# Kernel optimization log

Hardware: AMD Instinct MI355X
Metric: run time of the kernel (lower is better)

The kernel has to match this reference:

```python
import jax, jax.numpy as jnp
import numpy as np

D_MODEL = 1024
N_HEADS = 16
HEAD_DIM = D_MODEL // N_HEADS
B, LQ, LK = 4, 2048, 2048


def _rope(x, cos, sin):
    # x: (B, H, L, d); cos/sin: (B, 1, L, d)
    d = x.shape[-1]
    x1, x2 = x[..., : d // 2], x[..., d // 2 :]
    rotated = jnp.concatenate([-x2, x1], axis=-1)
    return x * cos + rotated * sin


def setup_inputs() -> dict:
    key = jax.random.key(0)
    ks = jax.random.split(key, 16)
    s = 1.0 / np.sqrt(D_MODEL)
    inp = {
        "query": jax.random.normal(ks[0], (B, LQ, D_MODEL), jnp.float32),
        "key": jax.random.normal(ks[1], (B, LK, D_MODEL), jnp.float32),
        "value": jax.random.normal(ks[2], (B, LK, D_MODEL), jnp.float32),
        "cos_q": jax.random.normal(ks[3], (B, LQ, HEAD_DIM), jnp.float32),
        "sin_q": jax.random.normal(ks[4], (B, LQ, HEAD_DIM), jnp.float32),
        "cos_k": jax.random.normal(ks[5], (B, LK, HEAD_DIM), jnp.float32),
        "sin_k": jax.random.normal(ks[6], (B, LK, HEAD_DIM), jnp.float32),
        "key_padding_mask": jnp.zeros((B, LK), dtype=bool),
        "Wq": jax.random.normal(ks[7], (D_MODEL, D_MODEL), jnp.float32) * s,
        "bq": jnp.zeros((D_MODEL,), jnp.float32),
        "Wk": jax.random.normal(ks[8], (D_MODEL, D_MODEL), jnp.float32) * s,
        "bk": jnp.zeros((D_MODEL,), jnp.float32),
        "Wv": jax.random.normal(ks[9], (D_MODEL, D_MODEL), jnp.float32) * s,
        "bv": jnp.zeros((D_MODEL,), jnp.float32),
        "Wo": jax.random.normal(ks[10], (D_MODEL, D_MODEL), jnp.float32) * s,
        "bo": jnp.zeros((D_MODEL,), jnp.float32),
    }
    return inp


def reference(query, key, value, cos_q, sin_q, cos_k, sin_k, key_padding_mask,
              Wq, bq, Wk, bk, Wv, bv, Wo, bo):
    Bq, Lq, _ = query.shape
    Lk = key.shape[1]
    scale = HEAD_DIM ** -0.5

    def proj(x, W, b, L):
        # torch Linear: x @ W.T + b, then (B, L, H, d) -> (B, H, L, d)
        y = jnp.einsum('ble,de->bld', x, W) + b
        return y.reshape(Bq, L, N_HEADS, HEAD_DIM).transpose(0, 2, 1, 3)

    q = proj(query, Wq, bq, Lq)
    k = proj(key, Wk, bk, Lk)
    v = proj(value, Wv, bv, Lk)

    q = _rope(q, cos_q[:, None, :Lq, :HEAD_DIM], sin_q[:, None, :Lq, :HEAD_DIM])
    k = _rope(k, cos_k[:, None, :Lk, :HEAD_DIM], sin_k[:, None, :Lk, :HEAD_DIM])

    attn = jnp.einsum('bhqd,bhkd->bhqk', q, k) * scale
    attn = jnp.where(key_padding_mask[:, None, None, :], -jnp.inf, attn)
    attn = jax.nn.softmax(attn, axis=-1)

    out = jnp.einsum('bhqk,bhkd->bhqd', attn, v)
    out = out.transpose(0, 2, 1, 3).reshape(Bq, Lq, D_MODEL)
    return jnp.einsum('ble,de->bld', out, Wo) + bo
```

## Files before the change

kernel.cpp:

```cpp
#include <hip/hip_runtime.h>
#include <hip/hip_bf16.h>
#include <stdint.h>
#include <stddef.h>

#define B_DIM 4
#define NH    16
#define LSEQ  2048
#define HD    64
#define DM    1024
#define TOKENS (B_DIM * LSEQ)

typedef __bf16 bf16_t;
typedef __attribute__((ext_vector_type(8))) __bf16 bf16x8;
typedef __attribute__((ext_vector_type(4))) __bf16 bf16x4;
typedef __attribute__((ext_vector_type(4))) float  f32x4;

#define GLD16(gp, lp) \
  __builtin_amdgcn_global_load_lds((__attribute__((address_space(1))) void*)(gp), \
                                   (__attribute__((address_space(3))) void*)(lp), 16, 0, 0)

#define WAITV4 asm volatile("s_waitcnt vmcnt(4)" ::: "memory")
#define WAITV0 asm volatile("s_waitcnt vmcnt(0)" ::: "memory")
#define WAITL0 asm volatile("s_waitcnt lgkmcnt(0)" ::: "memory")
#define SBAR   __builtin_amdgcn_s_barrier()
#define SCHED0 __builtin_amdgcn_sched_barrier(0)

__device__ __forceinline__ f32x4 mfma_16x16x32(bf16x8 a, bf16x8 b, f32x4 c) {
  return __builtin_amdgcn_mfma_f32_16x16x32_bf16(a, b, c, 0, 0, 0);
}

__global__ __launch_bounds__(256) void cast3_kernel(const float* __restrict__ a,
                                                    const float* __restrict__ b,
                                                    const float* __restrict__ c,
                                                    bf16_t* __restrict__ dst, int n) {
  const float* src = (blockIdx.y == 0) ? a : (blockIdx.y == 1) ? b : c;
  const int i = (blockIdx.x * 256 + threadIdx.x) * 4;
  if (i < n) {
    const float4 v = *(const float4*)(src + i);
    bf16x4 o;
    o[0] = (bf16_t)v.x; o[1] = (bf16_t)v.y; o[2] = (bf16_t)v.z; o[3] = (bf16_t)v.w;
    *(bf16x4*)(dst + (size_t)blockIdx.y * n + i) = o;
  }
}

__global__ __launch_bounds__(256) void cast4_kernel(const float* __restrict__ a,
                                                    const float* __restrict__ b,
                                                    const float* __restrict__ c,
                                                    const float* __restrict__ d,
                                                    bf16_t* __restrict__ dst, int n) {
  const float* src = (blockIdx.y == 0) ? a : (blockIdx.y == 1) ? b
                   : (blockIdx.y == 2) ? c : d;
  const int i = (blockIdx.x * 256 + threadIdx.x) * 4;
  if (i < n) {
    const float4 v = *(const float4*)(src + i);
    bf16x4 o;
    o[0] = (bf16_t)v.x; o[1] = (bf16_t)v.y; o[2] = (bf16_t)v.z; o[3] = (bf16_t)v.w;
    *(bf16x4*)(dst + (size_t)blockIdx.y * n + i) = o;
  }
}

#define GEMM_TILE(CUR, WAIT, PRE, KK2)                                        \
  {                                                                           \
    WAIT; SBAR; SCHED0;                                                       \
    const bf16_t* Ac = &As[CUR][0];                                           \
    const bf16_t* Bc = &Bs[CUR][0];                                           \
    bf16x8 af[4], bfr[4];                                                     \
    _Pragma("unroll") for (int i_ = 0; i_ < 4; ++i_)                          \
      af[i_] = *(const bf16x8*)(Ac + (wm + i_ * 16 + l16) * 32 + fcol);       \
    _Pragma("unroll") for (int j_ = 0; j_ < 4; ++j_)                          \
      bfr[j_] = *(const bf16x8*)(Bc + (wn + j_ * 16 + l16) * 32 + fcol);      \
    _Pragma("unroll") for (int i_ = 0; i_ < 4; ++i_)                          \
      _Pragma("unroll") for (int j_ = 0; j_ < 4; ++j_)                        \
        acc[i_][j_] = mfma_16x16x32(af[i_], bfr[j_], acc[i_][j_]);            \
    WAITL0; SBAR; SCHED0;                                                     \
    if (PRE) {                                                                \
      const int kk2_ = (KK2);                                                 \
      GLD16(Ag0 + kk2_, &As[CUR][0] + ld0);                                   \
      GLD16(Ag1 + kk2_, &As[CUR][0] + ld1);                                   \
      GLD16(Bg0 + kk2_, &Bs[CUR][0] + ld0);                                   \
      GLD16(Bg1 + kk2_, &Bs[CUR][0] + ld1);                                   \
    }                                                                         \
  }

__global__ __launch_bounds__(256) void qkv_proj_kernel(const bf16_t* __restrict__ X,
                                                       const bf16_t* __restrict__ Wb,
                                                       const float* __restrict__ bq,
                                                       const float* __restrict__ bk,
                                                       const float* __restrict__ bv,
                                                       const float* __restrict__ cos_q,
                                                       const float* __restrict__ sin_q,
                                                       const float* __restrict__ cos_k,
                                                       const float* __restrict__ sin_k,
                                                       bf16_t* __restrict__ qtb,
                                                       bf16_t* __restrict__ ktb,
                                                       bf16_t* __restrict__ vtb) {
  __shared__ bf16_t As[2][128 * 32];
  __shared__ bf16_t Bs[2][128 * 32];
  const int z = blockIdx.z;
  const bf16_t* A  = X  + (size_t)z * TOKENS * DM;
  const bf16_t* Bw = Wb + (size_t)z * DM * DM;
  const float* bias = (z == 0) ? bq : (z == 1) ? bk : bv;

  const int tid  = threadIdx.x;
  const int wave = tid >> 6, lane = tid & 63;
  const int quad = lane >> 4, l16 = lane & 15;
  const int m0 = blockIdx.x * 128, n0 = blockIdx.y * 128;
  const int wm = (wave >> 1) * 64, wn = (wave & 1) * 64;

  f32x4 acc[4][4];
#pragma unroll
  for (int i = 0; i < 4; ++i)
#pragma unroll
    for (int j = 0; j < 4; ++j) acc[i][j] = (f32x4){0.f, 0.f, 0.f, 0.f};

  const int srow = lane >> 2;
  const int scol = ((lane & 3) ^ ((lane >> 3) & 3)) * 8;
  const int c0 = wave * 2, c1 = c0 + 1;
  const int r0 = c0 * 16 + srow, r1 = c1 * 16 + srow;
  const bf16_t* Ag0 = A  + (size_t)(m0 + r0) * DM + scol;
  const bf16_t* Ag1 = A  + (size_t)(m0 + r1) * DM + scol;
  const bf16_t* Bg0 = Bw + (size_t)(n0 + r0) * DM + scol;
  const bf16_t* Bg1 = Bw + (size_t)(n0 + r1) * DM + scol;
  const int ld0 = c0 * 512, ld1 = c1 * 512;

  const int fcol = ((quad ^ ((l16 >> 1) & 3)) << 3);

  GLD16(Ag0, &As[0][0] + ld0); GLD16(Ag1, &As[0][0] + ld1);
  GLD16(Bg0, &Bs[0][0] + ld0); GLD16(Bg1, &Bs[0][0] + ld1);
  GLD16(Ag0 + 32, &As[1][0] + ld0); GLD16(Ag1 + 32, &As[1][0] + ld1);
  GLD16(Bg0 + 32, &Bs[1][0] + ld0); GLD16(Bg1 + 32, &Bs[1][0] + ld1);

  for (int ii = 0; ii < 15; ++ii) {
    const int kk2a = ii * 64 + 64;
    GEMM_TILE(0, WAITV4, true, kk2a);
    GEMM_TILE(1, WAITV4, true, kk2a + 32);
  }
  GEMM_TILE(0, WAITV4, false, 0);
  GEMM_TILE(1, WAITV0, false, 0);

  if (z < 2) {
    const float* cosb = (z == 0) ? cos_q : cos_k;
    const float* sinb = (z == 0) ? sin_q : sin_k;
    bf16_t* out = (z == 0) ? qtb : ktb;
    const int h = (n0 + wn) >> 6;
#pragma unroll
    for (int i = 0; i < 4; ++i) {
#pragma unroll
      for (int j = 0; j < 2; ++j) {
        const int hd1 = j * 16 + l16;
        const int hd2 = hd1 + 32;
        const float bn1 = bias[n0 + wn + hd1];
        const float bn2 = bias[n0 + wn + hd2];
#pragma unroll
        for (int r = 0; r < 4; ++r) {
          const int m = m0 + wm + i * 16 + quad * 4 + r;
          const int b = m >> 11, l = m & (LSEQ - 1);
          const size_t cb = ((size_t)b * LSEQ + l) * HD;
          const float x1 = (float)(bf16_t)(acc[i][j][r] + bn1);
          const float x2 = (float)(bf16_t)(acc[i][j + 2][r] + bn2);
          const float c1 = cosb[cb + hd1], s1 = sinb[cb + hd1];
          const float c2 = cosb[cb + hd2], s2 = sinb[cb + hd2];
          bf16_t* dst = out + (((size_t)(b * NH + h)) * LSEQ + l) * HD;
          dst[hd1] = (bf16_t)(x1 * c1 - x2 * s1);
          dst[hd2] = (bf16_t)(x2 * c2 + x1 * s2);
        }
      }
    }
  } else {
#pragma unroll
    for (int i = 0; i < 4; ++i) {
      const int mb = m0 + wm + i * 16 + quad * 4;
      const int b = mb >> 11, l = mb & (LSEQ - 1);
#pragma unroll
      for (int j = 0; j < 4; ++j) {
        const int n = n0 + wn + j * 16 + l16;
        const int h = n >> 6, hd = n & (HD - 1);
        const float bn = bias[n];
        bf16x4 pk;
#pragma unroll
        for (int r = 0; r < 4; ++r) pk[r] = (bf16_t)(acc[i][j][r] + bn);
        *(bf16x4*)(vtb + (((size_t)(b * NH + h)) * HD + hd) * LSEQ + l) = pk;
      }
    }
  }
}

__global__ __launch_bounds__(256) void out_gemm_kernel(const bf16_t* __restrict__ A,
                                                       const bf16_t* __restrict__ Bw,
                                                       const float* __restrict__ bias,
                                                       float* __restrict__ out) {
  __shared__ bf16_t As[2][128 * 32];
  __shared__ bf16_t Bs[2][128 * 32];
  const int tid  = threadIdx.x;
  const int wave = tid >> 6, lane = tid & 63;
  const int quad = lane >> 4, l16 = lane & 15;
  const int m0 = blockIdx.x * 128, n0 = blockIdx.y * 128;
  const int wm = (wave >> 1) * 64, wn = (wave & 1) * 64;

  f32x4 acc[4][4];
#pragma unroll
  for (int i = 0; i < 4; ++i)
#pragma unroll
    for (int j = 0; j < 4; ++j) acc[i][j] = (f32x4){0.f, 0.f, 0.f, 0.f};

  const int srow = lane >> 2;
  const int scol = ((lane & 3) ^ ((lane >> 3) & 3)) * 8;
  const int c0 = wave * 2, c1 = c0 + 1;
  const int r0 = c0 * 16 + srow, r1 = c1 * 16 + srow;
  const bf16_t* Ag0 = A  + (size_t)(m0 + r0) * DM + scol;
  const bf16_t* Ag1 = A  + (size_t)(m0 + r1) * DM + scol;
  const bf16_t* Bg0 = Bw + (size_t)(n0 + r0) * DM + scol;
  const bf16_t* Bg1 = Bw + (size_t)(n0 + r1) * DM + scol;
  const int ld0 = c0 * 512, ld1 = c1 * 512;
  const int fcol = ((quad ^ ((l16 >> 1) & 3)) << 3);

  GLD16(Ag0, &As[0][0] + ld0); GLD16(Ag1, &As[0][0] + ld1);
  GLD16(Bg0, &Bs[0][0] + ld0); GLD16(Bg1, &Bs[0][0] + ld1);
  GLD16(Ag0 + 32, &As[1][0] + ld0); GLD16(Ag1 + 32, &As[1][0] + ld1);
  GLD16(Bg0 + 32, &Bs[1][0] + ld0); GLD16(Bg1 + 32, &Bs[1][0] + ld1);

  for (int ii = 0; ii < 15; ++ii) {
    const int kk2a = ii * 64 + 64;
    GEMM_TILE(0, WAITV4, true, kk2a);
    GEMM_TILE(1, WAITV4, true, kk2a + 32);
  }
  GEMM_TILE(0, WAITV4, false, 0);
  GEMM_TILE(1, WAITV0, false, 0);

#pragma unroll
  for (int i = 0; i < 4; ++i)
#pragma unroll
    for (int j = 0; j < 4; ++j) {
      const int n  = n0 + wn + j * 16 + l16;
      const float bn = bias[n];
#pragma unroll
      for (int r = 0; r < 4; ++r) {
        const int m = m0 + wm + i * 16 + quad * 4 + r;
        out[(size_t)m * DM + n] = acc[i][j][r] + bn;
      }
    }
}

__global__ __launch_bounds__(256, 4) void attn_kernel(const bf16_t* __restrict__ qt,
                                                      const bf16_t* __restrict__ kt,
                                                      const bf16_t* __restrict__ vt,
                                                      const unsigned char* __restrict__ mask,
                                                      bf16_t* __restrict__ ctx) {
  __shared__ bf16_t Kl[2][64 * 64];
  __shared__ bf16_t Vl[2][64 * 64];
  __shared__ int mflag;
  const int bh = blockIdx.y;
  const int b = bh >> 4, h = bh & (NH - 1);
  const int q0 = blockIdx.x * 128;
  const int tid = threadIdx.x;
  const int wave = tid >> 6, lane = tid & 63;
  const int quad = lane >> 4, l16 = lane & 15;
  const float scale_l2e = 0.125f * 1.44269504f;

  const bf16_t* kbase = kt + (size_t)bh * LSEQ * HD;
  const bf16_t* vbase = vt + (size_t)bh * HD * LSEQ;
  const unsigned char* mrow = mask + (size_t)b * LSEQ;

  if (tid == 0) mflag = 0;
  __syncthreads();
  {
    const uint64_t mw = ((const uint64_t*)mrow)[tid];
    if (mw != 0) atomicOr(&mflag, 1);
  }

  bf16x8 qa[2][2];
#pragma unroll
  for (int u = 0; u < 2; ++u) {
    const bf16_t* qrow = qt + (((size_t)bh * LSEQ) + q0 + wave * 32 + u * 16 + l16) * HD;
    qa[u][0] = *(const bf16x8*)(qrow + quad * 8);
    qa[u][1] = *(const bf16x8*)(qrow + 32 + quad * 8);
  }

  f32x4 O[2][4];
  f32x4 Ol[2];
#pragma unroll
  for (int u = 0; u < 2; ++u) {
    Ol[u] = (f32x4){0.f, 0.f, 0.f, 0.f};
#pragma unroll
    for (int j = 0; j < 4; ++j) O[u][j] = (f32x4){0.f, 0.f, 0.f, 0.f};
  }
  bf16x8 ones;
#pragma unroll
  for (int e = 0; e < 8; ++e) ones[e] = (bf16_t)1.0f;

  const int srow8 = lane >> 3;
  const int scb   = lane & 7;
  const int c0 = wave * 2, c1 = c0 + 1;
  const int p0 = c0 * 8 + srow8, p1 = p0 + 8;
  const int g0 = (scb ^ srow8) * 8;
  const int sig0 = ((p0 >> 5) << 5) | (((p0 >> 2) & 3) << 3) | (((p0 >> 4) & 1) << 2) | (p0 & 3);
  const int sig1 = ((p1 >> 5) << 5) | (((p1 >> 2) & 3) << 3) | (((p1 >> 4) & 1) << 2) | (p1 & 3);
  const int kgo0 = sig0 * HD + g0, kgo1 = sig1 * HD + g0;
  const int vgo0 = p0 * LSEQ + g0, vgo1 = p1 * LSEQ + g0;
  const int ld0 = c0 * 512, ld1 = c1 * 512;

  const int sw  = l16 & 7;
  const int oA  = l16 * 64 + ((quad ^ sw) << 3);
  const int oB  = l16 * 64 + (((quad + 4) ^ sw) << 3);

  GLD16(kbase + kgo0, &Kl[0][0] + ld0);
  GLD16(kbase + kgo1, &Kl[0][0] + ld1);
  GLD16(vbase + vgo0, &Vl[0][0] + ld0);
  GLD16(vbase + vgo1, &Vl[0][0] + ld1);
  __syncthreads();
  const bool has_mask = (mflag != 0);

  int cur = 0;
  for (int t = 0; t < 32; ++t) {
    const int k0 = t * 64;

    if (t < 31) {
      const int k0n = k0 + 64;
      bf16_t* Kd = &Kl[cur ^ 1][0];
      bf16_t* Vd = &Vl[cur ^ 1][0];
      GLD16(kbase + (size_t)k0n * HD + kgo0, Kd + ld0);
      GLD16(kbase + (size_t)k0n * HD + kgo1, Kd + ld1);
      GLD16(vbase + (size_t)(vgo0 + k0n), Vd + ld0);
      GLD16(vbase + (size_t)(vgo1 + k0n), Vd + ld1);
    }

    const bf16_t* Kc = &Kl[cur][0];
    const bf16_t* Vc = &Vl[cur][0];

    f32x4 S[2][4];
#pragma unroll
    for (int j = 0; j < 4; ++j) {
      const bf16x8 kb0 = *(const bf16x8*)(Kc + oA + j * 1024);
      const bf16x8 kb1 = *(const bf16x8*)(Kc + oB + j * 1024);
#pragma unroll
      for (int u = 0; u < 2; ++u) {
        f32x4 a = (f32x4){0.f, 0.f, 0.f, 0.f};
        a = mfma_16x16x32(kb0, qa[u][0], a);
        a = mfma_16x16x32(kb1, qa[u][1], a);
#pragma unroll
        for (int r = 0; r < 4; ++r)
          S[u][j][r] = __builtin_amdgcn_exp2f(a[r] * scale_l2e);
      }
    }

    if (has_mask) {
      const uint64_t mlo = *(const uint64_t*)(mrow + k0 + quad * 8);
      const uint64_t mhi = *(const uint64_t*)(mrow + k0 + 32 + quad * 8);
      if (!__all((mlo | mhi) == 0)) {
#pragma unroll
        for (int j = 0; j < 4; ++j) {
          const uint64_t mm = (j & 2) ? mhi : mlo;
#pragma unroll
          for (int r = 0; r < 4; ++r)
            if ((mm >> (((j & 1) * 4 + r) * 8)) & 0xff) {
              S[0][j][r] = 0.f;
              S[1][j][r] = 0.f;
            }
        }
      }
    }

    bf16x8 pa[2][2];
#pragma unroll
    for (int u = 0; u < 2; ++u)
#pragma unroll
      for (int f = 0; f < 2; ++f)
#pragma unroll
        for (int e = 0; e < 8; ++e)
          pa[u][f][e] = (bf16_t)S[u][2 * f + (e >> 2)][e & 3];

#pragma unroll
    for (int u = 0; u < 2; ++u) {
      Ol[u] = mfma_16x16x32(pa[u][0], ones, Ol[u]);
      Ol[u] = mfma_16x16x32(pa[u][1], ones, Ol[u]);
    }

#pragma unroll
    for (int jd = 0; jd < 4; ++jd) {
      const bf16x8 vb0 = *(const bf16x8*)(Vc + oA + jd * 1024);
      const bf16x8 vb1 = *(const bf16x8*)(Vc + oB + jd * 1024);
#pragma unroll
      for (int u = 0; u < 2; ++u) {
        O[u][jd] = mfma_16x16x32(pa[u][0], vb0, O[u][jd]);
        O[u][jd] = mfma_16x16x32(pa[u][1], vb1, O[u][jd]);
      }
    }

    if (t < 31) __syncthreads();
    cur ^= 1;
  }

#pragma unroll
  for (int u = 0; u < 2; ++u) {
    f32x4 linv;
#pragma unroll
    for (int r = 0; r < 4; ++r) linv[r] = 1.0f / Ol[u][r];
#pragma unroll
    for (int jd = 0; jd < 4; ++jd)
#pragma unroll
      for (int r = 0; r < 4; ++r) {
        const int l = q0 + wave * 32 + u * 16 + quad * 4 + r;
        const int d = h * HD + jd * 16 + l16;
        const float o = O[u][jd][r] * linv[r];
        ctx[((size_t)b * LSEQ + l) * DM + d] = (bf16_t)o;
      }
  }
}

extern "C" void kernel_launch(void* const* d_in, const int* in_sizes, int n_in,
                              void* d_out, int out_size, void* d_ws, size_t ws_size,
                              hipStream_t stream) {
  (void)in_sizes; (void)n_in; (void)out_size; (void)ws_size;
  const float* query = (const float*)d_in[0];
  const float* key   = (const float*)d_in[1];
  const float* value = (const float*)d_in[2];
  const float* cos_q = (const float*)d_in[3];
  const float* sin_q = (const float*)d_in[4];
  const float* cos_k = (const float*)d_in[5];
  const float* sin_k = (const float*)d_in[6];
  const unsigned char* mask = (const unsigned char*)d_in[7];
  const float* Wq = (const float*)d_in[8];
  const float* bq = (const float*)d_in[9];
  const float* Wk = (const float*)d_in[10];
  const float* bk = (const float*)d_in[11];
  const float* Wv = (const float*)d_in[12];
  const float* bv = (const float*)d_in[13];
  const float* Wo = (const float*)d_in[14];
  const float* bo = (const float*)d_in[15];
  float* out = (float*)d_out;

  const size_t ACT = (size_t)TOKENS * DM;
  const size_t WEL = (size_t)DM * DM;

  bf16_t* p   = (bf16_t*)d_ws;
  bf16_t* xq  = p; p += ACT;
  bf16_t* xk  = p; p += ACT;
  bf16_t* xv  = p; p += ACT;
  bf16_t* wqb = p; p += WEL;
  bf16_t* wkb = p; p += WEL;
  bf16_t* wvb = p; p += WEL;
  bf16_t* wob = p; p += WEL;
  bf16_t* qtb = p; p += ACT;
  bf16_t* ktb = p; p += ACT;
  bf16_t* vtb = p; p += ACT;
  bf16_t* ctx = xk;
  (void)xv; (void)wkb; (void)wvb;

  cast3_kernel<<<dim3((int)(ACT / 1024), 3), 256, 0, stream>>>(query, key, value, xq, (int)ACT);
  cast4_kernel<<<dim3((int)(WEL / 1024), 4), 256, 0, stream>>>(Wq, Wk, Wv, Wo, wqb, (int)WEL);

  qkv_proj_kernel<<<dim3(TOKENS / 128, DM / 128, 3), 256, 0, stream>>>(
      xq, wqb, bq, bk, bv, cos_q, sin_q, cos_k, sin_k, qtb, ktb, vtb);

  attn_kernel<<<dim3(LSEQ / 128, B_DIM * NH), 256, 0, stream>>>(qtb, ktb, vtb, mask, ctx);

  out_gemm_kernel<<<dim3(TOKENS / 128, DM / 128), 256, 0, stream>>>(ctx, wob, bo, out);
}
```

Before: 359.9 us.

## Triple-buffer GEMM loads, swizzle block order, deepen attention prefetch pipeline

The projection GEMMs move from double to triple buffering in LDS with a vmcnt(8) wait, so global loads run two K-tiles ahead. Block indices in both GEMMs and the attention kernel are remapped so that neighbouring blocks share operand tiles in L2. The attention loop now prefetches two KV tiles ahead and uses explicit vmcnt waits and barriers in place of __syncthreads. The larger LDS footprint in the GEMMs may lower occupancy, and the remapping assumes fixed grid dimensions.

Measured after the change: 363.8 us. No clear change (+1.1%).

```diff
diff --git a/kernel.cpp b/kernel.cpp
--- a/kernel.cpp
+++ b/kernel.cpp
@@ -19,6 +19,7 @@
   __builtin_amdgcn_global_load_lds((__attribute__((address_space(1))) void*)(gp), \
                                    (__attribute__((address_space(3))) void*)(lp), 16, 0, 0)
 
+#define WAITV8 asm volatile("s_waitcnt vmcnt(8)" ::: "memory")
 #define WAITV4 asm volatile("s_waitcnt vmcnt(4)" ::: "memory")
 #define WAITV0 asm volatile("s_waitcnt vmcnt(0)" ::: "memory")
 #define WAITL0 asm volatile("s_waitcnt lgkmcnt(0)" ::: "memory")
@@ -82,6 +83,25 @@
     }                                                                         \
   }
 
+#define GEMM_LOOP                                                             \
+  GLD16(Ag0, &As[0][0] + ld0); GLD16(Ag1, &As[0][0] + ld1);                   \
+  GLD16(Bg0, &Bs[0][0] + ld0); GLD16(Bg1, &Bs[0][0] + ld1);                   \
+  GLD16(Ag0 + 32, &As[1][0] + ld0); GLD16(Ag1 + 32, &As[1][0] + ld1);         \
+  GLD16(Bg0 + 32, &Bs[1][0] + ld0); GLD16(Bg1 + 32, &Bs[1][0] + ld1);         \
+  GLD16(Ag0 + 64, &As[2][0] + ld0); GLD16(Ag1 + 64, &As[2][0] + ld1);         \
+  GLD16(Bg0 + 64, &Bs[2][0] + ld0); GLD16(Bg1 + 64, &Bs[2][0] + ld1);         \
+  for (int ii = 0; ii < 9; ++ii) {                                            \
+    const int kkb = ii * 96 + 96;                                             \
+    GEMM_TILE(0, WAITV8, true, kkb);                                          \
+    GEMM_TILE(1, WAITV8, true, kkb + 32);                                     \
+    GEMM_TILE(2, WAITV8, true, kkb + 64);                                     \
+  }                                                                           \
+  GEMM_TILE(0, WAITV8, true, 960);                                            \
+  GEMM_TILE(1, WAITV8, true, 992);                                            \
+  GEMM_TILE(2, WAITV8, false, 0);                                             \
+  GEMM_TILE(0, WAITV4, false, 0);                                             \
+  GEMM_TILE(1, WAITV0, false, 0);
+
 __global__ __launch_bounds__(256) void qkv_proj_kernel(const bf16_t* __restrict__ X,
                                                        const bf16_t* __restrict__ Wb,
                                                        const float* __restrict__ bq,
@@ -94,8 +114,8 @@
                                                        bf16_t* __restrict__ qtb,
                                                        bf16_t* __restrict__ ktb,
                                                        bf16_t* __restrict__ vtb) {
-  __shared__ bf16_t As[2][128 * 32];
-  __shared__ bf16_t Bs[2][128 * 32];
+  __shared__ bf16_t As[3][128 * 32];
+  __shared__ bf16_t Bs[3][128 * 32];
   const int z = blockIdx.z;
   const bf16_t* A  = X  + (size_t)z * TOKENS * DM;
   const bf16_t* Bw = Wb + (size_t)z * DM * DM;
@@ -104,7 +124,10 @@
   const int tid  = threadIdx.x;
   const int wave = tid >> 6, lane = tid & 63;
   const int quad = lane >> 4, l16 = lane & 15;
-  const int m0 = blockIdx.x * 128, n0 = blockIdx.y * 128;
+  const int L  = blockIdx.x + (blockIdx.y << 6);
+  const int mt = ((L & 7) << 3) | ((L >> 3) & 7);
+  const int nt = L >> 6;
+  const int m0 = mt * 128, n0 = nt * 128;
   const int wm = (wave >> 1) * 64, wn = (wave & 1) * 64;
 
   f32x4 acc[4][4];
@@ -125,18 +148,7 @@
 
   const int fcol = ((quad ^ ((l16 >> 1) & 3)) << 3);
 
-  GLD16(Ag0, &As[0][0] + ld0); GLD16(Ag1, &As[0][0] + ld1);
-  GLD16(Bg0, &Bs[0][0] + ld0); GLD16(Bg1, &Bs[0][0] + ld1);
-  GLD16(Ag0 + 32, &As[1][0] + ld0); GLD16(Ag1 + 32, &As[1][0] + ld1);
-  GLD16(Bg0 + 32, &Bs[1][0] + ld0); GLD16(Bg1 + 32, &Bs[1][0] + ld1);
-
-  for (int ii = 0; ii < 15; ++ii) {
-    const int kk2a = ii * 64 + 64;
-    GEMM_TILE(0, WAITV4, true, kk2a);
-    GEMM_TILE(1, WAITV4, true, kk2a + 32);
-  }
-  GEMM_TILE(0, WAITV4, false, 0);
-  GEMM_TILE(1, WAITV0, false, 0);
+  GEMM_LOOP
 
   if (z < 2) {
     const float* cosb = (z == 0) ? cos_q : cos_k;
@@ -189,12 +201,15 @@
                                                        const bf16_t* __restrict__ Bw,
                                                        const float* __restrict__ bias,
                                                        float* __restrict__ out) {
-  __shared__ bf16_t As[2][128 * 32];
-  __shared__ bf16_t Bs[2][128 * 32];
+  __shared__ bf16_t As[3][128 * 32];
+  __shared__ bf16_t Bs[3][128 * 32];
   const int tid  = threadIdx.x;
   const int wave = tid >> 6, lane = tid & 63;
   const int quad = lane >> 4, l16 = lane & 15;
-  const int m0 = blockIdx.x * 128, n0 = blockIdx.y * 128;
+  const int L  = blockIdx.x + (blockIdx.y << 6);
+  const int mt = ((L & 7) << 3) | ((L >> 3) & 7);
+  const int nt = L >> 6;
+  const int m0 = mt * 128, n0 = nt * 128;
   const int wm = (wave >> 1) * 64, wn = (wave & 1) * 64;
 
   f32x4 acc[4][4];
@@ -214,18 +229,7 @@
   const int ld0 = c0 * 512, ld1 = c1 * 512;
   const int fcol = ((quad ^ ((l16 >> 1) & 3)) << 3);
 
-  GLD16(Ag0, &As[0][0] + ld0); GLD16(Ag1, &As[0][0] + ld1);
-  GLD16(Bg0, &Bs[0][0] + ld0); GLD16(Bg1, &Bs[0][0] + ld1);
-  GLD16(Ag0 + 32, &As[1][0] + ld0); GLD16(Ag1 + 32, &As[1][0] + ld1);
-  GLD16(Bg0 + 32, &Bs[1][0] + ld0); GLD16(Bg1 + 32, &Bs[1][0] + ld1);
-
-  for (int ii = 0; ii < 15; ++ii) {
-    const int kk2a = ii * 64 + 64;
-    GEMM_TILE(0, WAITV4, true, kk2a);
-    GEMM_TILE(1, WAITV4, true, kk2a + 32);
-  }
-  GEMM_TILE(0, WAITV4, false, 0);
-  GEMM_TILE(1, WAITV0, false, 0);
+  GEMM_LOOP
 
 #pragma unroll
   for (int i = 0; i < 4; ++i)
@@ -240,6 +244,55 @@
       }
     }
 }
+
+#define ATTN_TILE(K0)                                                         \
+  {                                                                           \
+    const bf16_t* Kc = &Kl[cur][0];                                           \
+    const bf16_t* Vc = &Vl[cur][0];                                           \
+    f32x4 S[2][4];                                                            \
+    _Pragma("unroll") for (int j = 0; j < 4; ++j) {                           \
+      const bf16x8 kb0 = *(const bf16x8*)(Kc + oA + j * 1024);                \
+      const bf16x8 kb1 = *(const bf16x8*)(Kc + oB + j * 1024);                \
+      _Pragma("unroll") for (int u = 0; u < 2; ++u) {                         \
+        f32x4 a = (f32x4){0.f, 0.f, 0.f, 0.f};                                \
+        a = mfma_16x16x32(kb0, qa[u][0], a);                                  \
+        a = mfma_16x16x32(kb1, qa[u][1], a);                                  \
+        _Pragma("unroll") for (int r = 0; r < 4; ++r)                         \
+          S[u][j][r] = __builtin_amdgcn_exp2f(a[r] * scale_l2e);              \
+      }                                                                       \
+    }                                                                         \
+    if (has_mask) {                                                           \
+      const uint64_t mlo = *(const uint64_t*)(mrow + (K0) + quad * 8);        \
+      const uint64_t mhi = *(const uint64_t*)(mrow + (K0) + 32 + quad * 8);   \
+      if (!__all((mlo | mhi) == 0)) {                                         \
+        _Pragma("unroll") for (int j = 0; j < 4; ++j) {                       \
+          const uint64_t mm = (j & 2) ? mhi : mlo;                            \
+          _Pragma("unroll") for (int r = 0; r < 4; ++r)                       \
+            if ((mm >> (((j & 1) * 4 + r) * 8)) & 0xff) {                     \
+              S[0][j][r] = 0.f;                                               \
+              S[1][j][r] = 0.f;                                               \
+            }                                                                 \
+        }                                                                     \
+      }                                                                       \
+    }                                                                         \
+    bf16x8 pa[2][2];                                                          \
+    _Pragma("unroll") for (int u = 0; u < 2; ++u)                             \
+      _Pragma("unroll") for (int f = 0; f < 2; ++f)                           \
+        _Pragma("unroll") for (int e = 0; e < 8; ++e)                         \
+          pa[u][f][e] = (bf16_t)S[u][2 * f + (e >> 2)][e & 3];                \
+    _Pragma("unroll") for (int u = 0; u < 2; ++u) {                           \
+      Ol[u] = mfma_16x16x32(pa[u][0], ones, Ol[u]);                           \
+      Ol[u] = mfma_16x16x32(pa[u][1], ones, Ol[u]);                           \
+    }                                                                         \
+    _Pragma("unroll") for (int jd = 0; jd < 4; ++jd) {                        \
+      const bf16x8 vb0 = *(const bf16x8*)(Vc + oA + jd * 1024);               \
+      const bf16x8 vb1 = *(const bf16x8*)(Vc + oB + jd * 1024);               \
+      _Pragma("unroll") for (int u = 0; u < 2; ++u) {                         \
+        O[u][jd] = mfma_16x16x32(pa[u][0], vb0, O[u][jd]);                    \
+        O[u][jd] = mfma_16x16x32(pa[u][1], vb1, O[u][jd]);                    \
+      }                                                                       \
+    }                                                                         \
+  }
 
 __global__ __launch_bounds__(256, 4) void attn_kernel(const bf16_t* __restrict__ qt,
                                                       const bf16_t* __restrict__ kt,
@@ -249,9 +302,10 @@
   __shared__ bf16_t Kl[2][64 * 64];
   __shared__ bf16_t Vl[2][64 * 64];
   __shared__ int mflag;
-  const int bh = blockIdx.y;
+  const int L  = blockIdx.x + (blockIdx.y << 4);
+  const int bh = ((L & 7) << 3) | ((L >> 3) & 7);
+  const int q0 = (L >> 6) * 128;
   const int b = bh >> 4, h = bh & (NH - 1);
-  const int q0 = blockIdx.x * 128;
   const int tid = threadIdx.x;
   const int wave = tid >> 6, lane = tid & 63;
   const int quad = lane >> 4, l16 = lane & 15;
@@ -307,88 +361,35 @@
   GLD16(kbase + kgo1, &Kl[0][0] + ld1);
   GLD16(vbase + vgo0, &Vl[0][0] + ld0);
   GLD16(vbase + vgo1, &Vl[0][0] + ld1);
-  __syncthreads();
+  GLD16(kbase + (size_t)64 * HD + kgo0, &Kl[1][0] + ld0);
+  GLD16(kbase + (size_t)64 * HD + kgo1, &Kl[1][0] + ld1);
+  GLD16(vbase + (size_t)(vgo0 + 64), &Vl[1][0] + ld0);
+  GLD16(vbase + (size_t)(vgo1 + 64), &Vl[1][0] + ld1);
+
+  WAITL0; SBAR;
   const bool has_mask = (mflag != 0);
 
   int cur = 0;
-  for (int t = 0; t < 32; ++t) {
-    const int k0 = t * 64;
-
-    if (t < 31) {
-      const int k0n = k0 + 64;
-      bf16_t* Kd = &Kl[cur ^ 1][0];
-      bf16_t* Vd = &Vl[cur ^ 1][0];
+  for (int t = 0; t < 30; ++t) {
+    WAITV4; SBAR; SCHED0;
+    ATTN_TILE(t * 64);
+    WAITL0; SBAR; SCHED0;
+    {
+      const int k0n = t * 64 + 128;
+      bf16_t* Kd = &Kl[cur][0];
+      bf16_t* Vd = &Vl[cur][0];
       GLD16(kbase + (size_t)k0n * HD + kgo0, Kd + ld0);
       GLD16(kbase + (size_t)k0n * HD + kgo1, Kd + ld1);
       GLD16(vbase + (size_t)(vgo0 + k0n), Vd + ld0);
       GLD16(vbase + (size_t)(vgo1 + k0n), Vd + ld1);
     }
-
-    const bf16_t* Kc = &Kl[cur][0];
-    const bf16_t* Vc = &Vl[cur][0];
-
-    f32x4 S[2][4];
-#pragma unroll
-    for (int j = 0; j < 4; ++j) {
-      const bf16x8 kb0 = *(const bf16x8*)(Kc + oA + j * 1024);
-      const bf16x8 kb1 = *(const bf16x8*)(Kc + oB + j * 1024);
-#pragma unroll
-      for (int u = 0; u < 2; ++u) {
-        f32x4 a = (f32x4){0.f, 0.f, 0.f, 0.f};
-        a = mfma_16x16x32(kb0, qa[u][0], a);
-        a = mfma_16x16x32(kb1, qa[u][1], a);
-#pragma unroll
-        for (int r = 0; r < 4; ++r)
-          S[u][j][r] = __builtin_amdgcn_exp2f(a[r] * scale_l2e);
-      }
-    }
-
-    if (has_mask) {
-      const uint64_t mlo = *(const uint64_t*)(mrow + k0 + quad * 8);
-      const uint64_t mhi = *(const uint64_t*)(mrow + k0 + 32 + quad * 8);
-      if (!__all((mlo | mhi) == 0)) {
-#pragma unroll
-        for (int j = 0; j < 4; ++j) {
-          const uint64_t mm = (j & 2) ? mhi : mlo;
-#pragma unroll
-          for (int r = 0; r < 4; ++r)
-            if ((mm >> (((j & 1) * 4 + r) * 8)) & 0xff) {
-              S[0][j][r] = 0.f;
-              S[1][j][r] = 0.f;
-            }
-        }
-      }
-    }
-
-    bf16x8 pa[2][2];
-#pragma unroll
-    for (int u = 0; u < 2; ++u)
-#pragma unroll
-      for (int f = 0; f < 2; ++f)
-#pragma unroll
-        for (int e = 0; e < 8; ++e)
-          pa[u][f][e] = (bf16_t)S[u][2 * f + (e >> 2)][e & 3];
-
-#pragma unroll
-    for (int u = 0; u < 2; ++u) {
-      Ol[u] = mfma_16x16x32(pa[u][0], ones, Ol[u]);
-      Ol[u] = mfma_16x16x32(pa[u][1], ones, Ol[u]);
-    }
-
-#pragma unroll
-    for (int jd = 0; jd < 4; ++jd) {
-      const bf16x8 vb0 = *(const bf16x8*)(Vc + oA + jd * 1024);
-      const bf16x8 vb1 = *(const bf16x8*)(Vc + oB + jd * 1024);
-#pragma unroll
-      for (int u = 0; u < 2; ++u) {
-        O[u][jd] = mfma_16x16x32(pa[u][0], vb0, O[u][jd]);
-        O[u][jd] = mfma_16x16x32(pa[u][1], vb1, O[u][jd]);
-      }
-    }
-
-    if (t < 31) __syncthreads();
     cur ^= 1;
   }
+  WAITV4; SBAR; SCHED0;
+  ATTN_TILE(30 * 64);
+  cur ^= 1;
+  WAITV0; SBAR; SCHED0;
+  ATTN_TILE(31 * 64);
 
 #pragma unroll
   for (int u = 0; u < 2; ++u) {
```
